# Optimization experiments

Measured on AMD Instinct MI355X. Metric: run time of the kernel, lower is better.

## Reference

```python
import jax, jax.numpy as jnp
import numpy as np

GN_GROUPS = 32
GN_EPS = 1e-5


def _conv3x3(x, w, b):
    # NCHW 3x3 conv, stride 1, pad 1
    y = jax.lax.conv_general_dilated(x, w, (1, 1), [(1, 1), (1, 1)],
                                     dimension_numbers=('NCHW', 'OIHW', 'NCHW'))
    return y + b[None, :, None, None]


def _bilinear(x, py, px):
    # x: [N,C,H,W]; py,px: [N,H,W] fractional sample coords; zeros outside.
    N, C, H, W = x.shape
    y0 = jnp.floor(py)
    x0 = jnp.floor(px)
    wy = py - y0
    wx = px - x0
    xf = x.reshape(N, C, H * W)
    out = jnp.zeros((N, C, H, W), x.dtype)
    corners = ((y0, x0, (1 - wy) * (1 - wx)),
               (y0, x0 + 1, (1 - wy) * wx),
               (y0 + 1, x0, wy * (1 - wx)),
               (y0 + 1, x0 + 1, wy * wx))
    for yy, xx, w in corners:
        valid = ((yy >= 0) & (yy <= H - 1) & (xx >= 0) & (xx <= W - 1)).astype(x.dtype)
        yi = jnp.clip(yy, 0, H - 1).astype(jnp.int32)
        xi = jnp.clip(xx, 0, W - 1).astype(jnp.int32)
        idx = (yi * W + xi).reshape(N, 1, H * W)
        g = jnp.take_along_axis(xf, idx, axis=2).reshape(N, C, H, W)
        out = out + g * (w * valid)[:, None]
    return out


def setup_inputs() -> dict:
    key = jax.random.key(0)
    ks = jax.random.split(key, 8)
    N, C, H, W = 4, 128, 160, 160
    s = 0.05
    return {
        'x': jax.random.normal(ks[0], (N, C, H, W), jnp.float32),
        'w_tm': jax.random.normal(ks[1], (4, C, 3, 3), jnp.float32) * s,
        'b_tm': jax.random.normal(ks[2], (4,), jnp.float32) * s,
        'w_tr': jax.random.normal(ks[3], (2, C, 3, 3), jnp.float32) * s,
        'b_tr': jax.random.normal(ks[4], (2,), jnp.float32) * s,
        'w_dcn': jax.random.normal(ks[5], (C, C, 3, 3), jnp.float32) * s,
        'gn_gamma': jnp.ones((C,), jnp.float32),
        'gn_beta': jnp.zeros((C,), jnp.float32),
    }


def reference(x, w_tm, b_tm, w_tr, b_tr, w_dcn, gn_gamma, gn_beta):
    N, C, H, W = x.shape
    Cout = w_dcn.shape[0]
    # regular 3x3 grid offsets: row0 = ky, row1 = kx, k ordered ky-major
    R = jnp.array([[-1., -1., -1., 0., 0., 0., 1., 1., 1.],
                   [-1., 0., 1., -1., 0., 1., -1., 0., 1.]], x.dtype)
    tm = _conv3x3(x, w_tm, b_tm)   # [N,4,H,W] -> per-pixel 2x2 affine
    tr = _conv3x3(x, w_tr, b_tr)   # [N,2,H,W] -> per-pixel (dy,dx) translation
    tmm = tm.transpose(0, 2, 3, 1).reshape(N, H, W, 2, 2)
    off = jnp.einsum('nhwij,jk->nhwik', tmm, R) - R  # [N,H,W,2,9]
    dy = off[:, :, :, 0, :] + tr[:, 0][..., None]    # [N,H,W,9]
    dx = off[:, :, :, 1, :] + tr[:, 1][..., None]
    hh = jnp.arange(H, dtype=x.dtype)[None, :, None, None]
    ww = jnp.arange(W, dtype=x.dtype)[None, None, :, None]
    kk = jnp.arange(9)
    ky = (kk // 3).astype(x.dtype)
    kx = (kk % 3).astype(x.dtype)
    py = hh - 1.0 + ky + dy  # stride=1, pad=1, dilation=1
    px = ww - 1.0 + kx + dx
    wk = w_dcn.reshape(Cout, C, 9)
    out = jnp.zeros((N, Cout, H, W), x.dtype)
    for k in range(9):  # fixed small loop over kernel points
        s = _bilinear(x, py[..., k], px[..., k])
        out = out + jnp.einsum('nchw,oc->nohw', s, wk[:, :, k])
    # GroupNorm
    og = out.reshape(N, GN_GROUPS, (Cout // GN_GROUPS) * H * W)
    mu = og.mean(axis=2, keepdims=True)
    var = og.var(axis=2, keepdims=True)
    og = (og - mu) * jax.lax.rsqrt(var + GN_EPS)
    out = og.reshape(N, Cout, H, W) * gn_gamma[None, :, None, None] + gn_beta[None, :, None, None]
    return jax.nn.relu(out + x)
```

## Files before the change

### kernel.cpp

```cpp
#include <hip/hip_runtime.h>
#include <hip/hip_fp16.h>
#include <math.h>

#define Hh 160
#define Ww 160
#define Cc 128
#define HW 25600
#define NPIX 102400

typedef __attribute__((ext_vector_type(8))) _Float16 half8;
typedef __attribute__((ext_vector_type(4))) float f32x4;
typedef __attribute__((ext_vector_type(4))) unsigned int u32x4;

union h2u { __half2 h; unsigned int u; };

#define WS_OFFS 0u
#define WS_WA   7372800u
#define WS_GSUM 7667712u
#define WS_GSQ  7668224u
#define WS_XT   7668736u
#define WS_RAW  33883136u

__global__ void wtrans_kernel(const float* __restrict__ w_dcn,
                              unsigned short* __restrict__ wA) {
    int idx = blockIdx.x * 256 + threadIdx.x;
    if (idx >= 9 * 128 * 128) return;
    int k = idx >> 14;
    int o = (idx >> 7) & 127;
    int c = idx & 127;
    wA[idx] = __half_as_ushort(__float2half(w_dcn[(o * 128 + c) * 9 + k]));
}

__global__ void __launch_bounds__(256) xpose_kernel(
    const float* __restrict__ x, unsigned short* __restrict__ xT) {
    __shared__ float L[128 * 65];
    int b = blockIdx.x;
    int n = b / 400;
    int px0 = (b - n * 400) * 64;
    int t = threadIdx.x;
    const float* xn = x + (size_t)n * Cc * HW + px0;
#pragma unroll
    for (int i = 0; i < 32; ++i) {
        int idx = i * 256 + t;
        int ch = idx >> 6;
        int pxl = idx & 63;
        L[ch * 65 + pxl] = xn[(size_t)ch * HW + pxl];
    }
    __syncthreads();
    unsigned short* dst = xT + ((size_t)n * HW + px0) * 128;
#pragma unroll
    for (int j = 0; j < 16; ++j) {
        int idx = j * 256 + t;
        int pxl = idx >> 6;
        int cp = idx & 63;
        h2u cv;
        cv.h = __floats2half2_rn(L[(2 * cp) * 65 + pxl],
                                 L[(2 * cp + 1) * 65 + pxl]);
        *(unsigned int*)(dst + (size_t)pxl * 128 + cp * 2) = cv.u;
    }
}

__global__ void __launch_bounds__(256) offs_kernel(
    const float* __restrict__ x, const float* __restrict__ w_tm,
    const float* __restrict__ b_tm, const float* __restrict__ w_tr,
    const float* __restrict__ b_tr, float* __restrict__ offs2) {
    __shared__ float wt[128 * 9 * 8];
    int t = threadIdx.x;
    for (int idx = t; idx < 6912; idx += 256) {
        int j = idx % 6;
        int rest = idx / 6;
        int tap = rest % 9;
        int c = rest / 9;
        float v = (j < 4) ? w_tm[(j * 128 + c) * 9 + tap]
                          : w_tr[((j - 4) * 128 + c) * 9 + tap];
        wt[rest * 8 + j] = v;
    }
    __syncthreads();
    int bid = blockIdx.x;
    int blk = (bid & 7) * 50 + (bid >> 3);
    int p = blk * 256 + t;
    int n = p / HW;
    int hw = p - n * HW;
    int h = hw / Ww;
    int w = hw - h * Ww;
    int addr[9];
    float msk[9];
#pragma unroll
    for (int tap = 0; tap < 9; ++tap) {
        int dy = tap / 3 - 1, dx = tap % 3 - 1;
        int yy = h + dy, xx = w + dx;
        bool v = (yy >= 0) && (yy < Hh) && (xx >= 0) && (xx < Ww);
        addr[tap] = v ? yy * Ww + xx : 0;
        msk[tap] = v ? 1.f : 0.f;
    }
    float a0 = 0, a1 = 0, a2 = 0, a3 = 0, a4 = 0, a5 = 0;
    const float* xn = x + n * Cc * HW;
#pragma unroll 2
    for (int c = 0; c < Cc; ++c) {
        const float* xc = xn + c * HW;
#pragma unroll
        for (int tap = 0; tap < 9; ++tap) {
            float v = msk[tap] * xc[addr[tap]];
            const float* wp = &wt[(c * 9 + tap) * 8];
            float4 w4 = *(const float4*)wp;
            float2 w2 = *(const float2*)(wp + 4);
            a0 += v * w4.x; a1 += v * w4.y; a2 += v * w4.z; a3 += v * w4.w;
            a4 += v * w2.x; a5 += v * w2.y;
        }
    }
    a0 += b_tm[0]; a1 += b_tm[1]; a2 += b_tm[2]; a3 += b_tm[3];
    a4 += b_tr[0]; a5 += b_tr[1];
#pragma unroll
    for (int k = 0; k < 9; ++k) {
        float r0 = (float)(k / 3) - 1.f;
        float r1 = (float)(k % 3) - 1.f;
        float2 st;
        st.x = (float)h + a0 * r0 + a1 * r1 + a4;
        st.y = (float)w + a2 * r0 + a3 * r1 + a5;
        *(float2*)(offs2 + ((size_t)k * NPIX + p) * 2) = st;
    }
}

__global__ void __launch_bounds__(256, 5) dcn2_kernel(
    const unsigned short* __restrict__ xT, const float* __restrict__ offs2,
    const unsigned short* __restrict__ wA, float* __restrict__ raw,
    float* __restrict__ gsum, float* __restrict__ gsq) {
    __shared__ __align__(16) unsigned short Bt[2 * 64 * 128];
    int t = threadIdx.x;
    int lane = t & 63;
    int wid = t >> 6;
    int wm = wid & 1, wn = wid >> 1;
    int quad = lane >> 4, l15 = lane & 15;
    int sub = lane >> 4;
    int s = lane & 15;

    int bid = blockIdx.x;
    int blk = (bid & 7) * 200 + (bid >> 3);
    int px0 = blk * 64;
    int n = px0 / HW;
    int hw0 = px0 - n * HW;
    const unsigned short* xb = xT + (size_t)n * HW * 128;
    const char* Ag = (const char*)wA;
    const float2* offv = (const float2*)offs2;
    int pbase = px0 + wid * 16 + sub;
    int sb = s << 3;

    f32x4 acc[4][2];
#pragma unroll
    for (int i = 0; i < 4; ++i)
#pragma unroll
        for (int j = 0; j < 2; ++j) acc[i][j] = (f32x4)0.f;

    float2 pc[4], pcn[4];
    u32x4 v00[4], v01[4], v10[4], v11[4];
    float w00[4], w01[4], w10[4], w11[4];

    auto issue = [&]() {
#pragma unroll
        for (int r = 0; r < 4; ++r) {
            float py = pc[r].x, pxx = pc[r].y;
            float y0f = floorf(py), x0f = floorf(pxx);
            float fy = py - y0f, fx = pxx - x0f;
            int y0 = (int)y0f, xi0 = (int)x0f;
            int y1 = y0 + 1, xi1 = xi0 + 1;
            float a = (1.f - fy) * (1.f - fx), b = (1.f - fy) * fx;
            float c = fy * (1.f - fx), d = fy * fx;
            bool vy0 = (unsigned)y0 < (unsigned)Hh;
            bool vy1 = (unsigned)y1 < (unsigned)Hh;
            bool vx0 = (unsigned)xi0 < (unsigned)Ww;
            bool vx1 = (unsigned)xi1 < (unsigned)Ww;
            w00[r] = (vy0 && vx0) ? a : 0.f;
            w01[r] = (vy0 && vx1) ? b : 0.f;
            w10[r] = (vy1 && vx0) ? c : 0.f;
            w11[r] = (vy1 && vx1) ? d : 0.f;
            int cy0 = vy0 ? y0 : 0, cy1 = vy1 ? y1 : 0;
            int cx0 = vx0 ? xi0 : 0, cx1 = vx1 ? xi1 : 0;
            v00[r] = *(const u32x4*)(xb + ((size_t)(cy0 * Ww + cx0) << 7) + sb);
            v01[r] = *(const u32x4*)(xb + ((size_t)(cy0 * Ww + cx1) << 7) + sb);
            v10[r] = *(const u32x4*)(xb + ((size_t)(cy1 * Ww + cx0) << 7) + sb);
            v11[r] = *(const u32x4*)(xb + ((size_t)(cy1 * Ww + cx1) << 7) + sb);
        }
    };

    auto combine_write = [&](int bufbase) {
#pragma unroll
        for (int r = 0; r < 4; ++r) {
            int p = wid * 16 + r * 4 + sub;
            __half2 W00 = __float2half2_rn(w00[r]);
            __half2 W01 = __float2half2_rn(w01[r]);
            __half2 W10 = __float2half2_rn(w10[r]);
            __half2 W11 = __float2half2_rn(w11[r]);
            u32x4 outv;
#pragma unroll
            for (int e = 0; e < 4; ++e) {
                h2u a, b, c, d, o;
                a.u = v00[r][e]; b.u = v01[r][e]; c.u = v10[r][e]; d.u = v11[r][e];
                __half2 acc2 = __hmul2(W11, d.h);
                acc2 = __hfma2(W10, c.h, acc2);
                acc2 = __hfma2(W01, b.h, acc2);
                acc2 = __hfma2(W00, a.h, acc2);
                o.h = acc2;
                outv[e] = o.u;
            }
            *(u32x4*)&Bt[bufbase + p * 128 + ((s ^ (p & 15)) << 3)] = outv;
        }
    };

#pragma unroll
    for (int r = 0; r < 4; ++r) pc[r] = offv[pbase + r * 4];
    issue();
#pragma unroll
    for (int r = 0; r < 4; ++r) pc[r] = offv[(size_t)1 * NPIX + pbase + r * 4];
    combine_write(0);
    __syncthreads();

    for (int k = 0; k < 9; ++k) {
        int bufr = (k & 1) * (64 * 128);
        int bufw = ((k + 1) & 1) * (64 * 128);
        if (k < 7) {
#pragma unroll
            for (int r = 0; r < 4; ++r)
                pcn[r] = offv[(size_t)(k + 2) * NPIX + pbase + r * 4];
        }
        if (k < 8) issue();

#pragma unroll
        for (int q = 0; q < 4; ++q) {
            half8 a[4], b[2];
#pragma unroll
            for (int i = 0; i < 4; ++i)
                a[i] = *(const half8*)(Ag +
                        ((size_t)(k * 128 + wm * 64 + i * 16 + l15) << 8) +
                        q * 64 + quad * 16);
#pragma unroll
            for (int j = 0; j < 2; ++j) {
                int row = wn * 32 + j * 16 + l15;
                int ur = (q * 4 + quad) ^ (row & 15);
                b[j] = *(const half8*)&Bt[bufr + row * 128 + ur * 8];
            }
#pragma unroll
            for (int i = 0; i < 4; ++i)
#pragma unroll
                for (int j = 0; j < 2; ++j)
                    acc[i][j] = __builtin_amdgcn_mfma_f32_16x16x32_f16(
                        a[i], b[j], acc[i][j], 0, 0, 0);
        }

        if (k < 8) combine_write(bufw);
        __syncthreads();
        if (k < 7) {
#pragma unroll
            for (int r = 0; r < 4; ++r) pc[r] = pcn[r];
        }
    }

    size_t rbase = ((size_t)n * Cc) * HW + hw0;
#pragma unroll
    for (int i = 0; i < 4; ++i) {
        float s_i = 0.f, q_i = 0.f;
#pragma unroll
        for (int j = 0; j < 2; ++j) {
            int pxl = wn * 32 + j * 16 + l15;
#pragma unroll
            for (int rr = 0; rr < 4; ++rr) {
                int o = wm * 64 + i * 16 + quad * 4 + rr;
                float v = acc[i][j][rr];
                raw[rbase + (size_t)o * HW + pxl] = v;
                s_i += v;
                q_i += v * v;
            }
        }
#pragma unroll
        for (int m = 1; m < 16; m <<= 1) {
            s_i += __shfl_xor(s_i, m);
            q_i += __shfl_xor(q_i, m);
        }
        if (l15 == 0) {
            int g = wm * 16 + i * 4 + quad;
            atomicAdd(&gsum[n * 32 + g], s_i);
            atomicAdd(&gsq[n * 32 + g], q_i);
        }
    }
}

__global__ void __launch_bounds__(256) finish_kernel(
    const float* __restrict__ raw, const float* __restrict__ x,
    const float* __restrict__ gsum, const float* __restrict__ gsq,
    const float* __restrict__ gamma, const float* __restrict__ beta,
    float* __restrict__ out) {
    int i = blockIdx.x * 256 + threadIdx.x;
    int e = i * 4;
    int n = e / (Cc * HW);
    int rem = e - n * (Cc * HW);
    int c = rem / HW;
    int g = c >> 2;
    const float inv = 1.f / 102400.f;
    float mu = gsum[n * 32 + g] * inv;
    float var = gsq[n * 32 + g] * inv - mu * mu;
    float rs = rsqrtf(var + 1e-5f);
    float sc = gamma[c] * rs;
    float sh = beta[c] - mu * sc;
    float4 v = *(const float4*)&raw[e];
    float4 xv = *(const float4*)&x[e];
    float4 r;
    r.x = fmaxf(v.x * sc + sh + xv.x, 0.f);
    r.y = fmaxf(v.y * sc + sh + xv.y, 0.f);
    r.z = fmaxf(v.z * sc + sh + xv.z, 0.f);
    r.w = fmaxf(v.w * sc + sh + xv.w, 0.f);
    *(float4*)&out[e] = r;
}

extern "C" void kernel_launch(void* const* d_in, const int* in_sizes, int n_in,
                              void* d_out, int out_size, void* d_ws, size_t ws_size,
                              hipStream_t stream) {
    const float* x      = (const float*)d_in[0];
    const float* w_tm   = (const float*)d_in[1];
    const float* b_tm   = (const float*)d_in[2];
    const float* w_tr   = (const float*)d_in[3];
    const float* b_tr   = (const float*)d_in[4];
    const float* w_dcn  = (const float*)d_in[5];
    const float* gamma  = (const float*)d_in[6];
    const float* beta   = (const float*)d_in[7];
    char* ws = (char*)d_ws;
    float*          offs2 = (float*)(ws + WS_OFFS);
    unsigned short* wA    = (unsigned short*)(ws + WS_WA);
    float*          gsum  = (float*)(ws + WS_GSUM);
    float*          gsq   = (float*)(ws + WS_GSQ);
    unsigned short* xT    = (unsigned short*)(ws + WS_XT);
    float*          raw   = (float*)(ws + WS_RAW);
    float* out = (float*)d_out;

    (void)hipMemsetAsync(gsum, 0, 1024, stream);
    wtrans_kernel<<<576, 256, 0, stream>>>(w_dcn, wA);
    xpose_kernel<<<1600, 256, 0, stream>>>(x, xT);
    offs_kernel<<<400, 256, 0, stream>>>(x, w_tm, b_tm, w_tr, b_tr, offs2);
    dcn2_kernel<<<1600, 256, 0, stream>>>(xT, offs2, wA, raw, gsum, gsq);
    finish_kernel<<<12800, 256, 0, stream>>>(raw, x, gsum, gsq, gamma, beta, out);
}
```

Before: 399.9 us.

## Split bilinear gather into two halves interleaved with MFMA quads

The gather/combine of the next kernel tap is split into two halves of two rows each, interleaved with the four MFMA k-quads. This halves the live gather registers (v00..v11 from 4 to 2 slots). Launch bounds occupancy drops from 5 to 3 blocks per CU, which gives the compiler more registers and cuts spilling pressure. The risk is less memory latency hiding, because each half's loads have only two MFMA quads to overlap with, and there are fewer resident waves.

```diff
diff --git a/kernel.cpp b/kernel.cpp
--- a/kernel.cpp
+++ b/kernel.cpp
@@ -121,7 +121,7 @@
     }
 }
 
-__global__ void __launch_bounds__(256, 5) dcn2_kernel(
+__global__ void __launch_bounds__(256, 3) dcn2_kernel(
     const unsigned short* __restrict__ xT, const float* __restrict__ offs2,
     const unsigned short* __restrict__ wA, float* __restrict__ raw,
     float* __restrict__ gsum, float* __restrict__ gsq) {
@@ -152,66 +152,91 @@
         for (int j = 0; j < 2; ++j) acc[i][j] = (f32x4)0.f;
 
     float2 pc[4], pcn[4];
-    u32x4 v00[4], v01[4], v10[4], v11[4];
-    float w00[4], w01[4], w10[4], w11[4];
-
-    auto issue = [&]() {
-#pragma unroll
-        for (int r = 0; r < 4; ++r) {
-            float py = pc[r].x, pxx = pc[r].y;
-            float y0f = floorf(py), x0f = floorf(pxx);
-            float fy = py - y0f, fx = pxx - x0f;
-            int y0 = (int)y0f, xi0 = (int)x0f;
-            int y1 = y0 + 1, xi1 = xi0 + 1;
-            float a = (1.f - fy) * (1.f - fx), b = (1.f - fy) * fx;
-            float c = fy * (1.f - fx), d = fy * fx;
-            bool vy0 = (unsigned)y0 < (unsigned)Hh;
-            bool vy1 = (unsigned)y1 < (unsigned)Hh;
-            bool vx0 = (unsigned)xi0 < (unsigned)Ww;
-            bool vx1 = (unsigned)xi1 < (unsigned)Ww;
-            w00[r] = (vy0 && vx0) ? a : 0.f;
-            w01[r] = (vy0 && vx1) ? b : 0.f;
-            w10[r] = (vy1 && vx0) ? c : 0.f;
-            w11[r] = (vy1 && vx1) ? d : 0.f;
-            int cy0 = vy0 ? y0 : 0, cy1 = vy1 ? y1 : 0;
-            int cx0 = vx0 ? xi0 : 0, cx1 = vx1 ? xi1 : 0;
-            v00[r] = *(const u32x4*)(xb + ((size_t)(cy0 * Ww + cx0) << 7) + sb);
-            v01[r] = *(const u32x4*)(xb + ((size_t)(cy0 * Ww + cx1) << 7) + sb);
-            v10[r] = *(const u32x4*)(xb + ((size_t)(cy1 * Ww + cx0) << 7) + sb);
-            v11[r] = *(const u32x4*)(xb + ((size_t)(cy1 * Ww + cx1) << 7) + sb);
-        }
-    };
-
-    auto combine_write = [&](int bufbase) {
-#pragma unroll
-        for (int r = 0; r < 4; ++r) {
-            int p = wid * 16 + r * 4 + sub;
-            __half2 W00 = __float2half2_rn(w00[r]);
-            __half2 W01 = __float2half2_rn(w01[r]);
-            __half2 W10 = __float2half2_rn(w10[r]);
-            __half2 W11 = __float2half2_rn(w11[r]);
-            u32x4 outv;
-#pragma unroll
-            for (int e = 0; e < 4; ++e) {
-                h2u a, b, c, d, o;
-                a.u = v00[r][e]; b.u = v01[r][e]; c.u = v10[r][e]; d.u = v11[r][e];
-                __half2 acc2 = __hmul2(W11, d.h);
-                acc2 = __hfma2(W10, c.h, acc2);
-                acc2 = __hfma2(W01, b.h, acc2);
-                acc2 = __hfma2(W00, a.h, acc2);
-                o.h = acc2;
-                outv[e] = o.u;
-            }
-            *(u32x4*)&Bt[bufbase + p * 128 + ((s ^ (p & 15)) << 3)] = outv;
-        }
-    };
+    u32x4 v00[2], v01[2], v10[2], v11[2];
+    float w00[2], w01[2], w10[2], w11[2];
+
+#define ISSUE(sl, r) do {                                                   \
+    float py_ = pc[r].x, px_ = pc[r].y;                                     \
+    float y0f_ = floorf(py_), x0f_ = floorf(px_);                           \
+    float fy_ = py_ - y0f_, fx_ = px_ - x0f_;                               \
+    int y0_ = (int)y0f_, xi0_ = (int)x0f_;                                  \
+    int y1_ = y0_ + 1, xi1_ = xi0_ + 1;                                     \
+    float wa_ = (1.f - fy_) * (1.f - fx_), wb_ = (1.f - fy_) * fx_;         \
+    float wc_ = fy_ * (1.f - fx_), wd_ = fy_ * fx_;                         \
+    bool vy0_ = (unsigned)y0_ < (unsigned)Hh;                               \
+    bool vy1_ = (unsigned)y1_ < (unsigned)Hh;                               \
+    bool vx0_ = (unsigned)xi0_ < (unsigned)Ww;                              \
+    bool vx1_ = (unsigned)xi1_ < (unsigned)Ww;                              \
+    w00[sl] = (vy0_ && vx0_) ? wa_ : 0.f;                                   \
+    w01[sl] = (vy0_ && vx1_) ? wb_ : 0.f;                                   \
+    w10[sl] = (vy1_ && vx0_) ? wc_ : 0.f;                                   \
+    w11[sl] = (vy1_ && vx1_) ? wd_ : 0.f;                                   \
+    int cy0_ = vy0_ ? y0_ : 0, cy1_ = vy1_ ? y1_ : 0;                       \
+    int cx0_ = vx0_ ? xi0_ : 0, cx1_ = vx1_ ? xi1_ : 0;                     \
+    v00[sl] = *(const u32x4*)(xb + ((size_t)(cy0_ * Ww + cx0_) << 7) + sb); \
+    v01[sl] = *(const u32x4*)(xb + ((size_t)(cy0_ * Ww + cx1_) << 7) + sb); \
+    v10[sl] = *(const u32x4*)(xb + ((size_t)(cy1_ * Ww + cx0_) << 7) + sb); \
+    v11[sl] = *(const u32x4*)(xb + ((size_t)(cy1_ * Ww + cx1_) << 7) + sb); \
+} while (0)
+
+#define COMBINE(sl, r, bufbase) do {                                        \
+    int p_ = wid * 16 + (r) * 4 + sub;                                      \
+    __half2 W00_ = __float2half2_rn(w00[sl]);                               \
+    __half2 W01_ = __float2half2_rn(w01[sl]);                               \
+    __half2 W10_ = __float2half2_rn(w10[sl]);                               \
+    __half2 W11_ = __float2half2_rn(w11[sl]);                               \
+    u32x4 outv_;                                                            \
+    _Pragma("unroll")                                                       \
+    for (int e = 0; e < 4; ++e) {                                           \
+        h2u a_, b_, c_, d_, o_;                                             \
+        a_.u = v00[sl][e]; b_.u = v01[sl][e];                               \
+        c_.u = v10[sl][e]; d_.u = v11[sl][e];                               \
+        __half2 t_ = __hmul2(W11_, d_.h);                                   \
+        t_ = __hfma2(W10_, c_.h, t_);                                       \
+        t_ = __hfma2(W01_, b_.h, t_);                                       \
+        t_ = __hfma2(W00_, a_.h, t_);                                       \
+        o_.h = t_;                                                          \
+        outv_[e] = o_.u;                                                    \
+    }                                                                       \
+    *(u32x4*)&Bt[(bufbase) + p_ * 128 + ((s ^ (p_ & 15)) << 3)] = outv_;    \
+} while (0)
+
+#define MQUAD(q) do {                                                       \
+    half8 a0_, a1_, a2_, a3_, b0_, b1_;                                     \
+    a0_ = *(const half8*)(Ag + ((size_t)(k * 128 + wm * 64 + 0 + l15) << 8) \
+                          + (q) * 64 + quad * 16);                          \
+    a1_ = *(const half8*)(Ag + ((size_t)(k * 128 + wm * 64 + 16 + l15) << 8)\
+                          + (q) * 64 + quad * 16);                          \
+    a2_ = *(const half8*)(Ag + ((size_t)(k * 128 + wm * 64 + 32 + l15) << 8)\
+                          + (q) * 64 + quad * 16);                          \
+    a3_ = *(const half8*)(Ag + ((size_t)(k * 128 + wm * 64 + 48 + l15) << 8)\
+                          + (q) * 64 + quad * 16);                          \
+    {                                                                       \
+        int row0_ = wn * 32 + l15;                                          \
+        int row1_ = wn * 32 + 16 + l15;                                     \
+        int ur0_ = ((q) * 4 + quad) ^ (row0_ & 15);                         \
+        int ur1_ = ((q) * 4 + quad) ^ (row1_ & 15);                         \
+        b0_ = *(const half8*)&Bt[bufr + row0_ * 128 + ur0_ * 8];            \
+        b1_ = *(const half8*)&Bt[bufr + row1_ * 128 + ur1_ * 8];            \
+    }                                                                       \
+    acc[0][0] = __builtin_amdgcn_mfma_f32_16x16x32_f16(a0_, b0_, acc[0][0], 0, 0, 0); \
+    acc[0][1] = __builtin_amdgcn_mfma_f32_16x16x32_f16(a0_, b1_, acc[0][1], 0, 0, 0); \
+    acc[1][0] = __builtin_amdgcn_mfma_f32_16x16x32_f16(a1_, b0_, acc[1][0], 0, 0, 0); \
+    acc[1][1] = __builtin_amdgcn_mfma_f32_16x16x32_f16(a1_, b1_, acc[1][1], 0, 0, 0); \
+    acc[2][0] = __builtin_amdgcn_mfma_f32_16x16x32_f16(a2_, b0_, acc[2][0], 0, 0, 0); \
+    acc[2][1] = __builtin_amdgcn_mfma_f32_16x16x32_f16(a2_, b1_, acc[2][1], 0, 0, 0); \
+    acc[3][0] = __builtin_amdgcn_mfma_f32_16x16x32_f16(a3_, b0_, acc[3][0], 0, 0, 0); \
+    acc[3][1] = __builtin_amdgcn_mfma_f32_16x16x32_f16(a3_, b1_, acc[3][1], 0, 0, 0); \
+} while (0)
 
 #pragma unroll
     for (int r = 0; r < 4; ++r) pc[r] = offv[pbase + r * 4];
-    issue();
+    ISSUE(0, 0); ISSUE(1, 1);
+    COMBINE(0, 0, 0); COMBINE(1, 1, 0);
+    ISSUE(0, 2); ISSUE(1, 3);
+    COMBINE(0, 2, 0); COMBINE(1, 3, 0);
 #pragma unroll
     for (int r = 0; r < 4; ++r) pc[r] = offv[(size_t)1 * NPIX + pbase + r * 4];
-    combine_write(0);
     __syncthreads();
 
     for (int k = 0; k < 9; ++k) {
@@ -222,37 +247,24 @@
             for (int r = 0; r < 4; ++r)
                 pcn[r] = offv[(size_t)(k + 2) * NPIX + pbase + r * 4];
         }
-        if (k < 8) issue();
-
-#pragma unroll
-        for (int q = 0; q < 4; ++q) {
-            half8 a[4], b[2];
-#pragma unroll
-            for (int i = 0; i < 4; ++i)
-                a[i] = *(const half8*)(Ag +
-                        ((size_t)(k * 128 + wm * 64 + i * 16 + l15) << 8) +
-                        q * 64 + quad * 16);
-#pragma unroll
-            for (int j = 0; j < 2; ++j) {
-                int row = wn * 32 + j * 16 + l15;
-                int ur = (q * 4 + quad) ^ (row & 15);
-                b[j] = *(const half8*)&Bt[bufr + row * 128 + ur * 8];
-            }
-#pragma unroll
-            for (int i = 0; i < 4; ++i)
-#pragma unroll
-                for (int j = 0; j < 2; ++j)
-                    acc[i][j] = __builtin_amdgcn_mfma_f32_16x16x32_f16(
-                        a[i], b[j], acc[i][j], 0, 0, 0);
-        }
-
-        if (k < 8) combine_write(bufw);
+        if (k < 8) { ISSUE(0, 0); ISSUE(1, 1); }
+        MQUAD(0); MQUAD(1);
+        if (k < 8) {
+            COMBINE(0, 0, bufw); COMBINE(1, 1, bufw);
+            ISSUE(0, 2); ISSUE(1, 3);
+        }
+        MQUAD(2); MQUAD(3);
+        if (k < 8) { COMBINE(0, 2, bufw); COMBINE(1, 3, bufw); }
         __syncthreads();
         if (k < 7) {
 #pragma unroll
             for (int r = 0; r < 4; ++r) pc[r] = pcn[r];
         }
     }
+
+#undef ISSUE
+#undef COMBINE
+#undef MQUAD
 
     size_t rbase = ((size_t)n * Cc) * HW + hw0;
 #pragma unroll
```

Measured after the change: 400.8 us. Within noise of the previous version (+0.2%).
